# Optimization experiments

Hardware: AMD Instinct MI355X
Metric: run time of the kernel (lower is better)

Reference implementation:

```python
import jax, jax.numpy as jnp
import numpy as np

N = 2048        # num_nodes
E = 32768       # num input edges (avg degree 16)
F = 8           # edge feature dim
E_MAX = 1_048_576  # static padding for output edge count (expected ~525K two-hop + 32K orig)


def setup_inputs() -> dict:
    key = jax.random.key(0)
    k1, k2, k3 = jax.random.split(key, 3)
    src = jax.random.randint(k1, (E,), 0, N, dtype=jnp.int32)
    dst = jax.random.randint(k2, (E,), 0, N, dtype=jnp.int32)
    edge_index = jnp.stack([src, dst])                     # [2, E]
    edge_attr = jax.random.normal(k3, (E, F), dtype=jnp.float32)
    return {"num_nodes": N, "edge_index": edge_index, "edge_attr": edge_attr}


def reference(num_nodes, edge_index, edge_attr):
    n = num_nodes
    f = edge_attr.shape[1]
    src, dst = edge_index[0], edge_index[1]

    # to_torch_coo_tensor: adjacency with ones. Dense stand-in for SpGEMM.
    A = jnp.zeros((n, n), jnp.float32).at[src, dst].set(1.0)   # presence (input assumed coalesced)
    A2 = A @ A                                                  # path counts; structure of adj @ adj

    # remove_self_loops on the two-hop edges
    mask2 = (A2 > 0) & (~jnp.eye(n, dtype=bool))

    # original edge mask
    orig = jnp.zeros((n, n), dtype=bool).at[src, dst].set(True)

    # coalesce: union of edge sets, sorted lexicographically by (row, col).
    combined = orig | mask2

    # coalesce reduce='sum': duplicates of original edges sum their attrs;
    # two-hop-only edges contribute zeros (edge_attr2 = new_zeros).
    attr_dense = jnp.zeros((n, n, f), edge_attr.dtype).at[src, dst].add(edge_attr)

    # row-major nonzero == lexicographic (row, col) sort; static size via padding.
    rows, cols = jnp.nonzero(combined, size=E_MAX, fill_value=0)
    count = combined.sum()
    valid = jnp.arange(E_MAX) < count

    out_edge_index = jnp.stack([
        jnp.where(valid, rows, -1),
        jnp.where(valid, cols, -1),
    ]).astype(jnp.int32)                                        # [2, E_MAX], -1 padded
    out_attr = attr_dense[rows, cols] * valid[:, None]          # [E_MAX, F], zero padded
    return out_edge_index, out_attr
```

## Files before the change

kernel.cpp:

```cpp
#include <hip/hip_runtime.h>

#define N_NODES 2048
#define WORDS   64
#define E_MAX_OUT 1048576
#define FDIM    8


__global__ void __launch_bounds__(256) k_fill_build(const int* __restrict__ ei, int E,
                                                    float* __restrict__ out,
                                                    unsigned* __restrict__ a_bits) {
    int b = blockIdx.x;
    int t = threadIdx.x;

    int e = b * 256 + t;
    if (e < E) {
        int s = ei[e];
        int d = ei[E + e];
        atomicOr(&a_bits[s * WORDS + (d >> 5)], 1u << (d & 31));
    }

    const int TOTAL4 = (2 * E_MAX_OUT + FDIM * E_MAX_OUT) / 4;
    const int NEG4   = (2 * E_MAX_OUT) / 4;
    float4* o4 = (float4*)out;
    for (int p = b * 256 + t; p < TOTAL4; p += 2048 * 256) {
        float v = (p < NEG4) ? -1.0f : 0.0f;
        o4[p] = make_float4(v, v, v, v);
    }
}

__global__ void __launch_bounds__(256) k_twohop(const unsigned* __restrict__ a_bits,
                                                unsigned* __restrict__ c_bits,
                                                int* __restrict__ rel_off,
                                                int* __restrict__ row_cnt) {
    int lane = threadIdx.x & 63;
    int wv   = threadIdx.x >> 6;
    int i    = blockIdx.x * 4 + wv;
    __shared__ int nbr[4][256];
    __shared__ int ncnt_sh[4];

    unsigned r = a_bits[i * WORDS + lane];
    int pc = __popc(r);
    int incl = pc;
    for (int off = 1; off < 64; off <<= 1) {
        int v = __shfl_up(incl, off, 64);
        if (lane >= off) incl += v;
    }
    int base = incl - pc;
    unsigned bits = r;
    int wb = lane << 5;
    while (bits) {
        int b = __ffs(bits) - 1;
        bits &= bits - 1;
        nbr[wv][base++] = wb + b;
    }
    if (lane == 63) ncnt_sh[wv] = incl;
    __syncthreads();

    int nc = ncnt_sh[wv];
    const int* nb = nbr[wv];
    unsigned acc = 0u;
    int j = 0;
    for (; j + 4 <= nc; j += 4) {
        unsigned x0 = a_bits[nb[j]     * WORDS + lane];
        unsigned x1 = a_bits[nb[j + 1] * WORDS + lane];
        unsigned x2 = a_bits[nb[j + 2] * WORDS + lane];
        unsigned x3 = a_bits[nb[j + 3] * WORDS + lane];
        acc |= (x0 | x1) | (x2 | x3);
    }
    for (; j < nc; ++j) acc |= a_bits[nb[j] * WORDS + lane];

    if (lane == (i >> 5)) acc &= ~(1u << (i & 31));
    acc |= r;
    c_bits[i * WORDS + lane] = acc;

    int cnt = __popc(acc);
    int incl2 = cnt;
    for (int off = 1; off < 64; off <<= 1) {
        int v = __shfl_up(incl2, off, 64);
        if (lane >= off) incl2 += v;
    }
    rel_off[i * WORDS + lane] = incl2 - cnt;
    if (lane == 63) row_cnt[i] = incl2;
}

__global__ void __launch_bounds__(128) k3_emit(const unsigned* __restrict__ c_bits,
                                               const int* __restrict__ rel_off,
                                               const int* __restrict__ row_cnt,
                                               const int* __restrict__ ei,
                                               const float* __restrict__ attr, int E,
                                               float* __restrict__ out) {
    int i    = blockIdx.x;
    int t    = threadIdx.x;
    int lane = t & 63;
    int wv   = t >> 6;
    __shared__ int s_roff[N_NODES];
    __shared__ int s_cols[N_NODES];
    __shared__ int wsum[2];

    int vbase = t * (N_NODES / 128);
    int v16[N_NODES / 128];
    int s = 0;
    #pragma unroll
    for (int q = 0; q < N_NODES / 128; ++q) { v16[q] = row_cnt[vbase + q]; s += v16[q]; }
    int sincl = s;
    for (int off = 1; off < 64; off <<= 1) {
        int v = __shfl_up(sincl, off, 64);
        if (lane >= off) sincl += v;
    }
    if (lane == 63) wsum[wv] = sincl;
    __syncthreads();
    int run = ((wv == 1) ? wsum[0] : 0) + sincl - s;
    #pragma unroll
    for (int q = 0; q < N_NODES / 128; ++q) { s_roff[vbase + q] = run; run += v16[q]; }
    __syncthreads();

    int row_off_i = s_roff[i];
    int cnt_i     = row_cnt[i];

    if (wv == 0) {
        unsigned c = c_bits[i * WORDS + lane];
        int base = rel_off[i * WORDS + lane];
        int wb = lane << 5;
        while (c) {
            int bb = __ffs(c) - 1;
            c &= c - 1;
            s_cols[base++] = wb + bb;
        }
    } else {
        float* oattr = out + 2 * E_MAX_OUT;
        int q = lane & 3;
        for (int e = i * 16 + (lane >> 2); e < E; e += N_NODES * 16) {
            int s2 = ei[e];
            int d  = ei[E + e];
            int dw = d >> 5;
            unsigned cw = c_bits[s2 * WORDS + dw];
            int p = s_roff[s2] + rel_off[s2 * WORDS + dw]
                  + __popc(cw & ((1u << (d & 31)) - 1u));
            atomicAdd(&oattr[(size_t)p * FDIM + 2 * q],     attr[(size_t)e * FDIM + 2 * q]);
            atomicAdd(&oattr[(size_t)p * FDIM + 2 * q + 1], attr[(size_t)e * FDIM + 2 * q + 1]);
        }
    }
    __syncthreads();

    float fi = (float)i;
    for (int j = t; j < cnt_i; j += 128) {
        int p = row_off_i + j;
        out[p]             = fi;
        out[E_MAX_OUT + p] = (float)s_cols[j];
    }
}

extern "C" void kernel_launch(void* const* d_in, const int* in_sizes, int n_in,
                              void* d_out, int out_size, void* d_ws, size_t ws_size,
                              hipStream_t stream) {
    const int*   ei   = (const int*)d_in[1];
    const float* attr = (const float*)d_in[2];
    int E = in_sizes[1] / 2;

    float* out = (float*)d_out;
    unsigned char* ws = (unsigned char*)d_ws;
    unsigned* a_bits  = (unsigned*)(ws);
    unsigned* c_bits  = (unsigned*)(ws + 512 * 1024);
    int*      rel_off = (int*)(ws + 1024 * 1024);
    int*      row_cnt = (int*)(ws + 1536 * 1024);

    hipMemsetAsync(a_bits, 0, N_NODES * WORDS * sizeof(unsigned), stream);
    k_fill_build<<<2048, 256, 0, stream>>>(ei, E, out, a_bits);
    k_twohop    <<<N_NODES / 4, 256, 0, stream>>>(a_bits, c_bits, rel_off, row_cnt);
    k3_emit     <<<N_NODES, 128, 0, stream>>>(c_bits, rel_off, row_cnt, ei, attr, E, out);
}
```

Baseline: 29.83 us.

## Fill -1 index padding only past the valid count in emit kernel

The first kernel now zeroes only the attribute region of the output and no longer writes -1 over the whole index region. The emit kernel, widened to 256 threads, computes the total edge count and writes -1 padding only to index slots past that count, so valid entries are no longer written twice. This reduces redundant global writes but moves padding stores into the final kernel and adds a scalar tail loop in block 0. Edge bit-building is also spread across blocks at 16 edges per block.

```diff
diff --git a/kernel.cpp b/kernel.cpp
--- a/kernel.cpp
+++ b/kernel.cpp
@@ -7,25 +7,24 @@
 
 
 __global__ void __launch_bounds__(256) k_fill_build(const int* __restrict__ ei, int E,
-                                                    float* __restrict__ out,
+                                                    float* __restrict__ oattr,
                                                     unsigned* __restrict__ a_bits) {
     int b = blockIdx.x;
     int t = threadIdx.x;
 
-    int e = b * 256 + t;
-    if (e < E) {
-        int s = ei[e];
-        int d = ei[E + e];
-        atomicOr(&a_bits[s * WORDS + (d >> 5)], 1u << (d & 31));
+    if (t < 16) {
+        int e = b * 16 + t;
+        if (e < E) {
+            int s = ei[e];
+            int d = ei[E + e];
+            atomicOr(&a_bits[s * WORDS + (d >> 5)], 1u << (d & 31));
+        }
     }
 
-    const int TOTAL4 = (2 * E_MAX_OUT + FDIM * E_MAX_OUT) / 4;
-    const int NEG4   = (2 * E_MAX_OUT) / 4;
-    float4* o4 = (float4*)out;
-    for (int p = b * 256 + t; p < TOTAL4; p += 2048 * 256) {
-        float v = (p < NEG4) ? -1.0f : 0.0f;
-        o4[p] = make_float4(v, v, v, v);
-    }
+    const int A4 = FDIM * E_MAX_OUT / 4;
+    float4* o4 = (float4*)oattr;
+    float4 z = make_float4(0.f, 0.f, 0.f, 0.f);
+    for (int p = b * 256 + t; p < A4; p += 2048 * 256) o4[p] = z;
 }
 
 __global__ void __launch_bounds__(256) k_twohop(const unsigned* __restrict__ a_bits,
@@ -83,7 +82,7 @@
     if (lane == 63) row_cnt[i] = incl2;
 }
 
-__global__ void __launch_bounds__(128) k3_emit(const unsigned* __restrict__ c_bits,
+__global__ void __launch_bounds__(256) k3_emit(const unsigned* __restrict__ c_bits,
                                                const int* __restrict__ rel_off,
                                                const int* __restrict__ row_cnt,
                                                const int* __restrict__ ei,
@@ -95,13 +94,13 @@
     int wv   = t >> 6;
     __shared__ int s_roff[N_NODES];
     __shared__ int s_cols[N_NODES];
-    __shared__ int wsum[2];
+    __shared__ int wsum[4];
 
-    int vbase = t * (N_NODES / 128);
-    int v16[N_NODES / 128];
+    int vbase = t * (N_NODES / 256);
+    int v8[N_NODES / 256];
     int s = 0;
     #pragma unroll
-    for (int q = 0; q < N_NODES / 128; ++q) { v16[q] = row_cnt[vbase + q]; s += v16[q]; }
+    for (int q = 0; q < N_NODES / 256; ++q) { v8[q] = row_cnt[vbase + q]; s += v8[q]; }
     int sincl = s;
     for (int off = 1; off < 64; off <<= 1) {
         int v = __shfl_up(sincl, off, 64);
@@ -109,9 +108,12 @@
     }
     if (lane == 63) wsum[wv] = sincl;
     __syncthreads();
-    int run = ((wv == 1) ? wsum[0] : 0) + sincl - s;
+    int woff = 0;
+    for (int w = 0; w < wv; ++w) woff += wsum[w];
+    int run = woff + sincl - s;
     #pragma unroll
-    for (int q = 0; q < N_NODES / 128; ++q) { s_roff[vbase + q] = run; run += v16[q]; }
+    for (int q = 0; q < N_NODES / 256; ++q) { s_roff[vbase + q] = run; run += v8[q]; }
+    int count = wsum[0] + wsum[1] + wsum[2] + wsum[3];
     __syncthreads();
 
     int row_off_i = s_roff[i];
@@ -126,7 +128,7 @@
             c &= c - 1;
             s_cols[base++] = wb + bb;
         }
-    } else {
+    } else if (wv == 1) {
         float* oattr = out + 2 * E_MAX_OUT;
         int q = lane & 3;
         for (int e = i * 16 + (lane >> 2); e < E; e += N_NODES * 16) {
@@ -143,10 +145,26 @@
     __syncthreads();
 
     float fi = (float)i;
-    for (int j = t; j < cnt_i; j += 128) {
+    for (int j = t; j < cnt_i; j += 256) {
         int p = row_off_i + j;
         out[p]             = fi;
         out[E_MAX_OUT + p] = (float)s_cols[j];
+    }
+
+    int abase = (count + 3) & ~3;
+    if (i == 0) {
+        for (int p = count + t; p < abase; p += 256) {
+            out[p]             = -1.0f;
+            out[E_MAX_OUT + p] = -1.0f;
+        }
+    }
+    float4 m4 = make_float4(-1.f, -1.f, -1.f, -1.f);
+    float4* r4 = (float4*)out;
+    float4* c4 = (float4*)(out + E_MAX_OUT);
+    const int Q1 = E_MAX_OUT / 4;
+    for (int q = abase / 4 + i * 256 + t; q < Q1; q += N_NODES * 256) {
+        r4[q] = m4;
+        c4[q] = m4;
     }
 }
 
@@ -165,7 +183,7 @@
     int*      row_cnt = (int*)(ws + 1536 * 1024);
 
     hipMemsetAsync(a_bits, 0, N_NODES * WORDS * sizeof(unsigned), stream);
-    k_fill_build<<<2048, 256, 0, stream>>>(ei, E, out, a_bits);
+    k_fill_build<<<2048, 256, 0, stream>>>(ei, E, out + 2 * E_MAX_OUT, a_bits);
     k_twohop    <<<N_NODES / 4, 256, 0, stream>>>(a_bits, c_bits, rel_off, row_cnt);
-    k3_emit     <<<N_NODES, 128, 0, stream>>>(c_bits, rel_off, row_cnt, ei, attr, E, out);
+    k3_emit     <<<N_NODES, 256, 0, stream>>>(c_bits, rel_off, row_cnt, ei, attr, E, out);
 }
```

After: 29.65 us. No clear change (-0.6%).
